# Kernel tuning notes

Measured on AMD Instinct MI355X. Metric: run time of the kernel, lower is better.

Reference implementation:

```python
import jax, jax.numpy as jnp
import numpy as np

D_MODEL = 128; D_STATE = 64; D_CONV = 4; EXPAND = 2; HEADDIM = 32; NGROUPS = 1
D_INNER = EXPAND * D_MODEL            # 256
NHEADS = D_INNER // HEADDIM           # 8
CONV_DIM = D_INNER + 2 * NGROUPS * D_STATE   # 384 (x, B, C streams)
D_IN_PROJ = 2 * D_INNER + 2 * NGROUPS * D_STATE + NHEADS  # 648 (z, xBC, dt)
EPS = 1e-5


def setup_inputs() -> dict:
    key = jax.random.key(0)
    ks = jax.random.split(key, 8)
    B, L = 8, 4096
    x = jax.random.normal(ks[0], (B, L, D_MODEL), jnp.float32)
    norm_w = jnp.ones((D_MODEL,), jnp.float32)
    in_proj_w = jax.random.normal(ks[1], (D_IN_PROJ, D_MODEL), jnp.float32) * (D_MODEL ** -0.5)
    conv_w = jax.random.normal(ks[2], (CONV_DIM, D_CONV), jnp.float32) * (D_CONV ** -0.5)
    conv_b = jnp.zeros((CONV_DIM,), jnp.float32)
    dt_bias = jax.random.uniform(ks[3], (NHEADS,), jnp.float32, -4.0, -1.0)
    A_log = jnp.log(jax.random.uniform(ks[4], (NHEADS,), jnp.float32, 1.0, 16.0))
    D = jnp.ones((NHEADS,), jnp.float32)
    gnorm_w = jnp.ones((D_INNER,), jnp.float32)
    out_proj_w = jax.random.normal(ks[5], (D_MODEL, D_INNER), jnp.float32) * (D_INNER ** -0.5)
    return dict(x=x, norm_w=norm_w, in_proj_w=in_proj_w, conv_w=conv_w, conv_b=conv_b,
                dt_bias=dt_bias, A_log=A_log, D=D, gnorm_w=gnorm_w, out_proj_w=out_proj_w)


def _rmsnorm(x, w):
    return x * jax.lax.rsqrt(jnp.mean(x * x, axis=-1, keepdims=True) + EPS) * w


def _causal_dw_conv(x, w, b):
    # x: [B,L,C]; w: [C,K]; depthwise causal conv along L
    K = w.shape[1]
    xp = jnp.pad(x, ((0, 0), (K - 1, 0), (0, 0)))
    kern = jnp.transpose(w)[:, None, :]  # [K,1,C] for WIO with groups=C
    out = jax.lax.conv_general_dilated(
        xp, kern, window_strides=(1,), padding='VALID',
        dimension_numbers=('NWC', 'WIO', 'NWC'),
        feature_group_count=w.shape[0])
    return out + b


def _ssm(xh, dt, Bm, Cm, A):
    # xh: [B,L,H,P]; dt: [B,L,H]; Bm, Cm: [B,L,N]; A: [H]
    def step(h, inp):
        x_t, dt_t, B_t, C_t = inp
        dA = jnp.exp(dt_t * A)                                   # [B,H]
        h = h * dA[..., None, None] + (dt_t[..., None] * x_t)[..., None] * B_t[:, None, None, :]
        y = jnp.einsum('bhpn,bn->bhp', h, C_t)
        return h, y
    Bsz, L, H, P = xh.shape
    N = Bm.shape[-1]
    h0 = jnp.zeros((Bsz, H, P, N), xh.dtype)
    xs = (xh.transpose(1, 0, 2, 3), dt.transpose(1, 0, 2),
          Bm.transpose(1, 0, 2), Cm.transpose(1, 0, 2))
    _, ys = jax.lax.scan(step, h0, xs)
    return ys.transpose(1, 0, 2, 3)  # [B,L,H,P]


def reference(x, norm_w, in_proj_w, conv_w, conv_b, dt_bias, A_log, D, gnorm_w, out_proj_w):
    xn = _rmsnorm(x, norm_w)
    zxbcdt = xn @ in_proj_w.T                                    # [B,L,648]
    z, xBC, dt = jnp.split(zxbcdt, [D_INNER, D_INNER + CONV_DIM], axis=-1)
    dt = jax.nn.softplus(dt + dt_bias)                           # [B,L,H]
    xBC = jax.nn.silu(_causal_dw_conv(xBC, conv_w, conv_b))
    xs, Bm, Cm = jnp.split(xBC, [D_INNER, D_INNER + NGROUPS * D_STATE], axis=-1)
    Bsz, L, _ = x.shape
    xh = xs.reshape(Bsz, L, NHEADS, HEADDIM)
    A = -jnp.exp(A_log)                                          # [H]
    y = _ssm(xh, dt, Bm, Cm, A) + D[None, None, :, None] * xh    # D skip per head
    y = y.reshape(Bsz, L, D_INNER)
    y = _rmsnorm(y * jax.nn.silu(z), gnorm_w)                    # gated RMSNorm
    out = y @ out_proj_w.T
    return x + out
```

## Files before the change

### kernel.cpp

```cpp
#include <hip/hip_runtime.h>

#define DM    128
#define DI    256
#define NH    8
#define HD    32
#define NS    64
#define CDIM  384
#define DPROJ 648
#define LSEQ  4096
#define NB    8
#define NTOK  32768
#define LC    64
#define NC    64
#define EPSF  1e-5f
#define LOG2E 1.4426950408889634f

typedef __bf16 bf16;
typedef bf16  bf16x8 __attribute__((ext_vector_type(8)));
typedef bf16  bf16x4 __attribute__((ext_vector_type(4)));
typedef short short8 __attribute__((ext_vector_type(8)));
typedef float f32x4  __attribute__((ext_vector_type(4)));

__device__ __forceinline__ unsigned short f2bfbits(float f) {
    unsigned int u = __float_as_uint(f);
    unsigned int r = u + 0x7FFFu + ((u >> 16) & 1u);
    return (unsigned short)(r >> 16);
}
__device__ __forceinline__ float bfbits2f(unsigned short u) {
    return __uint_as_float(((unsigned int)u) << 16);
}

__global__ __launch_bounds__(256) void k_cast(const float* __restrict__ in,
                                              unsigned short* __restrict__ out, int n) {
    int i = blockIdx.x * 256 + threadIdx.x;
    if (i < n) out[i] = f2bfbits(in[i]);
}

__global__ __launch_bounds__(256) void k_rmsdt(const float* __restrict__ x,
                                               const float* __restrict__ w,
                                               const float* __restrict__ w1,
                                               const float* __restrict__ dtb,
                                               unsigned short* __restrict__ xnb,
                                               float* __restrict__ dtf) {
    __shared__ float Xs[4][132];
    __shared__ float Wd[8][132];
    const int t = threadIdx.x;
    {
        int row = t >> 5, col = (t & 31) * 4;
        *(float4*)&Wd[row][col] = *(const float4*)(w1 + (size_t)(640 + row) * DM + col);
    }
    const int wave = t >> 6, lane = t & 63;
    const size_t row = (size_t)blockIdx.x * 4 + wave;
    const float* xr = x + row * DM + lane * 2;
    float v0 = xr[0], v1 = xr[1];
    float ss = v0 * v0 + v1 * v1;
    #pragma unroll
    for (int o = 32; o; o >>= 1) ss += __shfl_xor(ss, o);
    float r = rsqrtf(ss * (1.0f / DM) + EPSF);
    float o0 = v0 * r * w[lane * 2], o1 = v1 * r * w[lane * 2 + 1];
    Xs[wave][lane * 2] = o0; Xs[wave][lane * 2 + 1] = o1;
    ushort2 ob; ob.x = f2bfbits(o0); ob.y = f2bfbits(o1);
    *(ushort2*)(xnb + row * DM + lane * 2) = ob;
    __syncthreads();
    const int h = lane >> 3, ks = lane & 7;
    float acc = 0.f;
    #pragma unroll
    for (int i = 0; i < 4; i++) {
        float4 xv = *(const float4*)&Xs[wave][ks * 16 + i * 4];
        float4 wv = *(const float4*)&Wd[h][ks * 16 + i * 4];
        acc = fmaf(xv.x, wv.x, acc);
        acc = fmaf(xv.y, wv.y, acc);
        acc = fmaf(xv.z, wv.z, acc);
        acc = fmaf(xv.w, wv.w, acc);
    }
    acc += __shfl_xor(acc, 1);
    acc += __shfl_xor(acc, 2);
    acc += __shfl_xor(acc, 4);
    if (ks == 0) {
        float v = acc + dtb[h];
        dtf[row * NH + h] = (v > 20.f) ? v : log1pf(expf(v));
    }
}

__global__ __launch_bounds__(256) void k_gemm1(const unsigned short* __restrict__ A,
                                               const unsigned short* __restrict__ B,
                                               unsigned short* __restrict__ zb,
                                               unsigned short* __restrict__ xbc) {
    __shared__ bf16 As[64 * 40];
    __shared__ bf16 Bs[64 * 40];
    const int t = threadIdx.x;
    const int m0 = blockIdx.x * 64, n0 = blockIdx.y * 64;
    const int wave = t >> 6, lane = t & 63;
    const int wm = wave >> 1, wn = wave & 1;
    const int fr = lane & 15, fk = (lane >> 4) * 8;
    f32x4 acc[2][2] = {};
    const int r = t >> 2, q = (t & 3) * 8;
    for (int k0 = 0; k0 < DM; k0 += 32) {
        __syncthreads();
        *(short8*)&As[r * 40 + q] = *(const short8*)(A + (size_t)(m0 + r) * DM + k0 + q);
        short8 bv = {};
        if (n0 + r < DPROJ) bv = *(const short8*)(B + (size_t)(n0 + r) * DM + k0 + q);
        *(short8*)&Bs[r * 40 + q] = bv;
        __syncthreads();
        #pragma unroll
        for (int mt = 0; mt < 2; mt++) {
            bf16x8 af = *(const bf16x8*)&As[(wm * 32 + mt * 16 + fr) * 40 + fk];
            #pragma unroll
            for (int nt = 0; nt < 2; nt++) {
                bf16x8 bf = *(const bf16x8*)&Bs[(wn * 32 + nt * 16 + fr) * 40 + fk];
                acc[mt][nt] = __builtin_amdgcn_mfma_f32_16x16x32_bf16(af, bf, acc[mt][nt], 0, 0, 0);
            }
        }
    }
    #pragma unroll
    for (int mt = 0; mt < 2; mt++)
        #pragma unroll
        for (int nt = 0; nt < 2; nt++) {
            int n = n0 + wn * 32 + nt * 16 + fr;
            if (n >= 640) continue;
            #pragma unroll
            for (int rr = 0; rr < 4; rr++) {
                int m = m0 + wm * 32 + mt * 16 + (lane >> 4) * 4 + rr;
                unsigned short v = f2bfbits(acc[mt][nt][rr]);
                if (n < DI) zb[(size_t)m * DI + n] = v;
                else        xbc[(size_t)m * CDIM + (n - 256)] = v;
            }
        }
}

__global__ __launch_bounds__(384) void k_conv(const unsigned short* __restrict__ xbc,
                                              const float* __restrict__ cw,
                                              const float* __restrict__ cb,
                                              unsigned short* __restrict__ xcb) {
    const int c = threadIdx.x;
    const int t0 = blockIdx.x * 64;
    const int l0 = t0 & (LSEQ - 1);
    float4 wv = *(const float4*)(cw + c * 4);
    float bias = cb[c];
    const unsigned short* in = xbc + (size_t)t0 * CDIM + c;
    unsigned short* out = xcb + (size_t)t0 * CDIM + c;
    float h1 = 0.f, h2 = 0.f, h3 = 0.f;
    if (l0) {
        h1 = bfbits2f(in[-CDIM]);
        h2 = bfbits2f(in[-2 * CDIM]);
        h3 = bfbits2f(in[-3 * CDIM]);
    }
    #pragma unroll 4
    for (int t = 0; t < 64; t++) {
        float x0 = bfbits2f(in[(size_t)t * CDIM]);
        float acc = bias;
        acc = fmaf(x0, wv.w, acc);
        acc = fmaf(h1, wv.z, acc);
        acc = fmaf(h2, wv.y, acc);
        acc = fmaf(h3, wv.x, acc);
        float s = acc / (1.f + expf(-acc));
        out[(size_t)t * CDIM] = f2bfbits(s);
        h3 = h2; h2 = h1; h1 = x0;
    }
}

__global__ __launch_bounds__(256, 2) void k_ssd1(const unsigned short* __restrict__ xcb,
                                                 const float* __restrict__ dtf,
                                                 const float* __restrict__ alog,
                                                 unsigned short* __restrict__ hst,
                                                 float* __restrict__ dAp) {
    __shared__ bf16 Wl[4][64 * 72];
    __shared__ bf16 Xl[4][64 * 40];
    __shared__ float wl[4][64];
    const int bh = blockIdx.x >> 4, cg = blockIdx.x & 15;
    const int b = bh >> 3, h = bh & 7;
    const int wave = threadIdx.x >> 6, lane = threadIdx.x & 63;
    const int c = cg * 4 + wave;
    const size_t tok0 = (size_t)b * LSEQ + c * LC;
    const float A = -expf(alog[h]);
    float dt = dtf[(tok0 + lane) * NH + h];
    float q = dt * A * LOG2E;
    #pragma unroll
    for (int o = 1; o <= 32; o <<= 1) {
        float tmp = __shfl_up(q, o);
        if (lane >= o) q += tmp;
    }
    float qL = __shfl(q, 63);
    wl[wave][lane] = exp2f(qL - q) * dt;
    const unsigned short* xrow = xcb + tok0 * CDIM;
    #pragma unroll
    for (int it = 0; it < 4; it++) {
        int f = it * 64 + lane, r = f >> 2, c8 = (f & 3) * 8;
        *(bf16x8*)&Xl[wave][r * 40 + c8] = *(const bf16x8*)(xrow + (size_t)r * CDIM + h * HD + c8);
    }
    #pragma unroll
    for (int it = 0; it < 8; it++) {
        int f = it * 64 + lane, r = f >> 3, c8 = (f & 7) * 8;
        float w = wl[wave][r];
        bf16x8 v = *(const bf16x8*)(xrow + (size_t)r * CDIM + 256 + c8);
        bf16x8 o;
        #pragma unroll
        for (int j = 0; j < 8; j++) o[j] = (bf16)((float)v[j] * w);
        *(bf16x8*)&Wl[wave][r * 72 + c8] = o;
    }
    const int m = lane & 15, ko = lane >> 4;
    f32x4 hacc[4][2] = {};
    #pragma unroll
    for (int kh = 0; kh < 2; kh++) {
        bf16x8 xb[2];
        #pragma unroll
        for (int pi = 0; pi < 2; pi++)
            #pragma unroll
            for (int j = 0; j < 8; j++)
                xb[pi][j] = Xl[wave][(kh * 32 + ko * 8 + j) * 40 + pi * 16 + m];
        #pragma unroll
        for (int ni = 0; ni < 4; ni++) {
            bf16x8 af;
            #pragma unroll
            for (int j = 0; j < 8; j++)
                af[j] = Wl[wave][(kh * 32 + ko * 8 + j) * 72 + ni * 16 + m];
            #pragma unroll
            for (int pi = 0; pi < 2; pi++)
                hacc[ni][pi] = __builtin_amdgcn_mfma_f32_16x16x32_bf16(af, xb[pi], hacc[ni][pi], 0, 0, 0);
        }
    }
    unsigned short* hb = hst + (((size_t)bh * NC + c) << 11);
    #pragma unroll
    for (int ni = 0; ni < 4; ni++)
        #pragma unroll
        for (int pi = 0; pi < 2; pi++)
            #pragma unroll
            for (int r = 0; r < 4; r++)
                hb[(ni * 16 + ko * 4 + r) * 32 + pi * 16 + m] = f2bfbits(hacc[ni][pi][r]);
    if (lane == 0) dAp[(size_t)bh * NC + c] = exp2f(qL);
}

__global__ __launch_bounds__(256) void k_ssm2(unsigned short* __restrict__ hst,
                                              const float* __restrict__ dAp) {
    __shared__ float dl[2][NC];
    const int pr = blockIdx.x >> 3, seg = blockIdx.x & 7;
    const int bh0 = pr * 2, bh1 = pr * 2 + 1;
    const int s = seg * 256 + threadIdx.x;
    if (threadIdx.x < NC) dl[0][threadIdx.x] = dAp[(size_t)bh0 * NC + threadIdx.x];
    else if (threadIdx.x < 2 * NC) dl[1][threadIdx.x - NC] = dAp[(size_t)bh1 * NC + threadIdx.x - NC];
    __syncthreads();
    unsigned short* b0 = hst + ((size_t)bh0 * NC << 11) + s;
    unsigned short* b1 = hst + ((size_t)bh1 * NC << 11) + s;
    float r0 = 0.f, r1 = 0.f;
    float n0 = bfbits2f(b0[0]), n1 = bfbits2f(b1[0]);
    for (int c = 0; c < NC; c++) {
        float t0 = n0, t1 = n1;
        if (c + 1 < NC) {
            n0 = bfbits2f(b0[(size_t)(c + 1) << 11]);
            n1 = bfbits2f(b1[(size_t)(c + 1) << 11]);
        }
        b0[(size_t)c << 11] = f2bfbits(r0);
        b1[(size_t)c << 11] = f2bfbits(r1);
        r0 = fmaf(r0, dl[0][c], t0);
        r1 = fmaf(r1, dl[1][c], t1);
    }
}

__global__ __launch_bounds__(256, 2) void k_ssd3(const unsigned short* __restrict__ xcb,
                                                 const float* __restrict__ dtf,
                                                 const float* __restrict__ alog,
                                                 const unsigned short* __restrict__ hst,
                                                 const float* __restrict__ Dw,
                                                 unsigned short* __restrict__ ybb) {
    __shared__ bf16 Pl[4][64 * 72];
    __shared__ bf16 Xl[4][64 * 40];
    __shared__ bf16 Hl[4][64 * 40];
    __shared__ float ql[4][64];
    __shared__ float dl[4][64];
    const int bh = blockIdx.x >> 4, cg = blockIdx.x & 15;
    const int b = bh >> 3, h = bh & 7;
    const int wave = threadIdx.x >> 6, lane = threadIdx.x & 63;
    const int c = cg * 4 + wave;
    const size_t tok0 = (size_t)b * LSEQ + c * LC;
    const float A = -expf(alog[h]);
    const float Dh = Dw[h];
    float dt = dtf[(tok0 + lane) * NH + h];
    float q = dt * A * LOG2E;
    #pragma unroll
    for (int o = 1; o <= 32; o <<= 1) {
        float tmp = __shfl_up(q, o);
        if (lane >= o) q += tmp;
    }
    ql[wave][lane] = q;
    dl[wave][lane] = dt;
    const unsigned short* xrow = xcb + tok0 * CDIM;
    #pragma unroll
    for (int it = 0; it < 4; it++) {
        int f = it * 64 + lane, r = f >> 2, c8 = (f & 3) * 8;
        *(bf16x8*)&Xl[wave][r * 40 + c8] = *(const bf16x8*)(xrow + (size_t)r * CDIM + h * HD + c8);
    }
    const unsigned short* hbg = hst + (((size_t)bh * NC + c) << 11);
    #pragma unroll
    for (int it = 0; it < 4; it++) {
        int f = it * 64 + lane, n = f >> 2, p8 = (f & 3) * 8;
        *(bf16x8*)&Hl[wave][n * 40 + p8] = *(const bf16x8*)(hbg + f * 8);
    }
    const int m = lane & 15, ko = lane >> 4;
    bf16x8 cf[4][2];
    #pragma unroll
    for (int ti = 0; ti < 4; ti++)
        #pragma unroll
        for (int kh = 0; kh < 2; kh++)
            cf[ti][kh] = *(const bf16x8*)(xrow + (size_t)(ti * 16 + m) * CDIM + 320 + kh * 32 + ko * 8);
    f32x4 g[4][4] = {};
    #pragma unroll
    for (int kh = 0; kh < 2; kh++) {
        bf16x8 bfg[4];
        #pragma unroll
        for (int si = 0; si < 4; si++)
            bfg[si] = *(const bf16x8*)(xrow + (size_t)(si * 16 + m) * CDIM + 256 + kh * 32 + ko * 8);
        #pragma unroll
        for (int ti = 0; ti < 4; ti++)
            #pragma unroll
            for (int si = 0; si < 4; si++)
                g[ti][si] = __builtin_amdgcn_mfma_f32_16x16x32_bf16(cf[ti][kh], bfg[si], g[ti][si], 0, 0, 0);
    }
    __syncthreads();
    float qt[4][4], et[4][4];
    #pragma unroll
    for (int ti = 0; ti < 4; ti++)
        #pragma unroll
        for (int r = 0; r < 4; r++) {
            float v = ql[wave][ti * 16 + ko * 4 + r];
            qt[ti][r] = v; et[ti][r] = exp2f(v);
        }
    float qs[4], ds[4];
    #pragma unroll
    for (int si = 0; si < 4; si++) {
        qs[si] = ql[wave][si * 16 + m];
        ds[si] = dl[wave][si * 16 + m];
    }
    #pragma unroll
    for (int ti = 0; ti < 4; ti++)
        #pragma unroll
        for (int si = 0; si < 4; si++)
            #pragma unroll
            for (int r = 0; r < 4; r++) {
                int t = ti * 16 + ko * 4 + r, s = si * 16 + m;
                float p = 0.f;
                if (si <= ti) {
                    float w = (s <= t) ? exp2f(qt[ti][r] - qs[si]) * ds[si] : 0.f;
                    p = g[ti][si][r] * w;
                    if (s == t) p += Dh;
                }
                Pl[wave][t * 72 + s] = (bf16)p;
            }
    f32x4 ya[4][2] = {}, ua[4][2] = {};
    #pragma unroll
    for (int kh = 0; kh < 2; kh++) {
        bf16x8 xb[2], hb2[2];
        #pragma unroll
        for (int pi = 0; pi < 2; pi++)
            #pragma unroll
            for (int j = 0; j < 8; j++) {
                int kk = kh * 32 + ko * 8 + j;
                xb[pi][j]  = Xl[wave][kk * 40 + pi * 16 + m];
                hb2[pi][j] = Hl[wave][kk * 40 + pi * 16 + m];
            }
        #pragma unroll
        for (int ti = 0; ti < 4; ti++) {
            bf16x8 pa = *(const bf16x8*)&Pl[wave][(ti * 16 + m) * 72 + kh * 32 + ko * 8];
            #pragma unroll
            for (int pi = 0; pi < 2; pi++) {
                ya[ti][pi] = __builtin_amdgcn_mfma_f32_16x16x32_bf16(pa, xb[pi], ya[ti][pi], 0, 0, 0);
                ua[ti][pi] = __builtin_amdgcn_mfma_f32_16x16x32_bf16(cf[ti][kh], hb2[pi], ua[ti][pi], 0, 0, 0);
            }
        }
    }
    unsigned short* yrow = ybb + tok0 * DI + h * HD;
    #pragma unroll
    for (int ti = 0; ti < 4; ti++)
        #pragma unroll
        for (int pi = 0; pi < 2; pi++)
            #pragma unroll
            for (int r = 0; r < 4; r++) {
                int t = ti * 16 + ko * 4 + r;
                yrow[(size_t)t * DI + pi * 16 + m] =
                    f2bfbits(ya[ti][pi][r] + et[ti][r] * ua[ti][pi][r]);
            }
}

__global__ __launch_bounds__(256, 2) void k_gemm2g(const unsigned short* __restrict__ ybb,
                                                   const unsigned short* __restrict__ zb,
                                                   const float* __restrict__ gw,
                                                   const unsigned short* __restrict__ w2b,
                                                   const float* __restrict__ xin,
                                                   float* __restrict__ out) {
    __shared__ bf16 Ws[128 * 264];
    __shared__ float gwl[256];
    const int t = threadIdx.x;
    #pragma unroll
    for (int i = 0; i < 16; i++) {
        int f = i * 256 + t;
        int n = f >> 5, u = (f & 31) * 8;
        *(bf16x8*)&Ws[n * 264 + u] = *(const bf16x8*)(w2b + (size_t)n * DI + u);
    }
    gwl[t] = gw[t];
    const int wave = t >> 6, lane = t & 63;
    const int fr = lane & 15, ko = lane >> 4;
    const int m0 = blockIdx.x * 64 + wave * 16;
    const size_t rowo = (size_t)(m0 + fr) * DI;
    float ss = 0.f;
    bf16x8 gb[8];
    #pragma unroll
    for (int kk = 0; kk < 8; kk++) {
        int co = kk * 32 + ko * 8;
        bf16x8 yv = *(const bf16x8*)(ybb + rowo + co);
        bf16x8 zv = *(const bf16x8*)(zb + rowo + co);
        #pragma unroll
        for (int j = 0; j < 8; j++) {
            float z = (float)zv[j];
            float g = (float)yv[j] * (z / (1.f + expf(-z)));
            ss += g * g;
            gb[kk][j] = (bf16)g;
        }
    }
    ss += __shfl_xor(ss, 16);
    ss += __shfl_xor(ss, 32);
    const float rs = rsqrtf(ss * (1.0f / DI) + EPSF);
    __syncthreads();
    #pragma unroll
    for (int kk = 0; kk < 8; kk++) {
        int co = kk * 32 + ko * 8;
        #pragma unroll
        for (int j = 0; j < 8; j++)
            gb[kk][j] = (bf16)((float)gb[kk][j] * rs * gwl[co + j]);
    }
    f32x4 acc[8] = {};
    #pragma unroll
    for (int kk = 0; kk < 8; kk++) {
        #pragma unroll
        for (int nt = 0; nt < 8; nt++) {
            bf16x8 bfr = *(const bf16x8*)&Ws[(nt * 16 + fr) * 264 + kk * 32 + ko * 8];
            acc[nt] = __builtin_amdgcn_mfma_f32_16x16x32_bf16(gb[kk], bfr, acc[nt], 0, 0, 0);
        }
    }
    #pragma unroll
    for (int nt = 0; nt < 8; nt++) {
        int n = nt * 16 + fr;
        #pragma unroll
        for (int rr = 0; rr < 4; rr++) {
            int m = m0 + ko * 4 + rr;
            out[(size_t)m * DM + n] = xin[(size_t)m * DM + n] + acc[nt][rr];
        }
    }
}

extern "C" void kernel_launch(void* const* d_in, const int* in_sizes, int n_in,
                              void* d_out, int out_size, void* d_ws, size_t ws_size,
                              hipStream_t stream) {
    const float* x   = (const float*)d_in[0];
    const float* nw  = (const float*)d_in[1];
    const float* w1  = (const float*)d_in[2];
    const float* cw  = (const float*)d_in[3];
    const float* cb  = (const float*)d_in[4];
    const float* dtb = (const float*)d_in[5];
    const float* al  = (const float*)d_in[6];
    const float* Dw  = (const float*)d_in[7];
    const float* gw  = (const float*)d_in[8];
    const float* w2  = (const float*)d_in[9];
    float* out = (float*)d_out;

    float* ws = (float*)d_ws;
    float*  dAp = ws;
    float*  dtf = dAp + NB * NH * NC;
    unsigned short* hst = (unsigned short*)(dtf + (size_t)NTOK * NH);
    unsigned short* zb  = hst + (size_t)NB * NH * NC * 2048;
    unsigned short* xbc = zb + (size_t)NTOK * DI;
    unsigned short* xcb = xbc + (size_t)NTOK * CDIM;
    unsigned short* ybb = xcb + (size_t)NTOK * CDIM;
    unsigned short* w1b = ybb + (size_t)NTOK * DI;
    unsigned short* w2b = w1b + (size_t)DPROJ * DM;
    unsigned short* xnb = ybb;

    k_cast<<<(DPROJ * DM + 255) / 256, 256, 0, stream>>>(w1, w1b, DPROJ * DM);
    k_cast<<<(DM * DI + 255) / 256, 256, 0, stream>>>(w2, w2b, DM * DI);
    k_rmsdt<<<NTOK / 4, 256, 0, stream>>>(x, nw, w1, dtb, xnb, dtf);
    k_gemm1<<<dim3(NTOK / 64, (DPROJ + 63) / 64), 256, 0, stream>>>(xnb, w1b, zb, xbc);
    k_conv<<<NTOK / 64, 384, 0, stream>>>(xbc, cw, cb, xcb);
    k_ssd1<<<NB * NH * (NC / 4), 256, 0, stream>>>(xcb, dtf, al, hst, dAp);
    k_ssm2<<<(NB * NH / 2) * 8, 256, 0, stream>>>(hst, dAp);
    k_ssd3<<<NB * NH * (NC / 4), 256, 0, stream>>>(xcb, dtf, al, hst, Dw, ybb);
    k_gemm2g<<<NTOK / 64, 256, 0, stream>>>(ybb, zb, gw, w2b, x, out);
}
```

Baseline: 193.1 us.

## Emit transposed conv outputs so SSD kernels load MFMA fragments directly

The conv kernel now writes its output in three layouts: a compact B/C token-major buffer, and channel-major (transposed) x and B buffers staged through shared memory. The SSD chunk kernels then load MFMA operands as contiguous vectors straight from global memory, no longer staging through LDS with scalar transposed reads, so ssd1 can raise occupancy. ssd3 computes the transposed Gram matrix so the P tile is written as packed vectors. The two weight-cast launches are merged and gemm1 drops its N-bound checks by launching exactly 10 column tiles. The conv kernel does more work and writes more bytes in exchange.

```diff
diff --git a/kernel.cpp b/kernel.cpp
--- a/kernel.cpp
+++ b/kernel.cpp
@@ -30,10 +30,17 @@
     return __uint_as_float(((unsigned int)u) << 16);
 }
 
-__global__ __launch_bounds__(256) void k_cast(const float* __restrict__ in,
-                                              unsigned short* __restrict__ out, int n) {
+__global__ __launch_bounds__(256) void k_cast2(const float* __restrict__ a,
+                                               const float* __restrict__ b,
+                                               unsigned short* __restrict__ oa,
+                                               unsigned short* __restrict__ ob,
+                                               int na, int nb) {
     int i = blockIdx.x * 256 + threadIdx.x;
-    if (i < n) out[i] = f2bfbits(in[i]);
+    if (i < na) oa[i] = f2bfbits(a[i]);
+    else {
+        int j = i - na;
+        if (j < nb) ob[j] = f2bfbits(b[j]);
+    }
 }
 
 __global__ __launch_bounds__(256) void k_rmsdt(const float* __restrict__ x,
@@ -98,9 +105,7 @@
     for (int k0 = 0; k0 < DM; k0 += 32) {
         __syncthreads();
         *(short8*)&As[r * 40 + q] = *(const short8*)(A + (size_t)(m0 + r) * DM + k0 + q);
-        short8 bv = {};
-        if (n0 + r < DPROJ) bv = *(const short8*)(B + (size_t)(n0 + r) * DM + k0 + q);
-        *(short8*)&Bs[r * 40 + q] = bv;
+        *(short8*)&Bs[r * 40 + q] = *(const short8*)(B + (size_t)(n0 + r) * DM + k0 + q);
         __syncthreads();
         #pragma unroll
         for (int mt = 0; mt < 2; mt++) {
@@ -117,7 +122,6 @@
         #pragma unroll
         for (int nt = 0; nt < 2; nt++) {
             int n = n0 + wn * 32 + nt * 16 + fr;
-            if (n >= 640) continue;
             #pragma unroll
             for (int rr = 0; rr < 4; rr++) {
                 int m = m0 + wm * 32 + mt * 16 + (lane >> 4) * 4 + rr;
@@ -131,21 +135,24 @@
 __global__ __launch_bounds__(384) void k_conv(const unsigned short* __restrict__ xbc,
                                               const float* __restrict__ cw,
                                               const float* __restrict__ cb,
-                                              unsigned short* __restrict__ xcb) {
+                                              unsigned short* __restrict__ bcA,
+                                              unsigned short* __restrict__ xT,
+                                              unsigned short* __restrict__ bT) {
+    __shared__ __align__(16) unsigned short L[320][72];
     const int c = threadIdx.x;
     const int t0 = blockIdx.x * 64;
     const int l0 = t0 & (LSEQ - 1);
     float4 wv = *(const float4*)(cw + c * 4);
     float bias = cb[c];
     const unsigned short* in = xbc + (size_t)t0 * CDIM + c;
-    unsigned short* out = xcb + (size_t)t0 * CDIM + c;
     float h1 = 0.f, h2 = 0.f, h3 = 0.f;
     if (l0) {
         h1 = bfbits2f(in[-CDIM]);
         h2 = bfbits2f(in[-2 * CDIM]);
         h3 = bfbits2f(in[-3 * CDIM]);
     }
-    #pragma unroll 4
+    short8 pk;
+    #pragma unroll 8
     for (int t = 0; t < 64; t++) {
         float x0 = bfbits2f(in[(size_t)t * CDIM]);
         float acc = bias;
@@ -154,19 +161,34 @@
         acc = fmaf(h2, wv.y, acc);
         acc = fmaf(h3, wv.x, acc);
         float s = acc / (1.f + expf(-acc));
-        out[(size_t)t * CDIM] = f2bfbits(s);
+        unsigned short us = f2bfbits(s);
+        if (c >= 256) bcA[(size_t)(t0 + t) * 128 + (c - 256)] = us;
+        pk[t & 7] = (short)us;
+        if (c < 320 && (t & 7) == 7) *(short8*)&L[c][t - 7] = pk;
         h3 = h2; h2 = h1; h1 = x0;
     }
-}
-
-__global__ __launch_bounds__(256, 2) void k_ssd1(const unsigned short* __restrict__ xcb,
+    __syncthreads();
+    #pragma unroll
+    for (int it = 0; it < 7; it++) {
+        int idx = it * 384 + c;
+        if (idx < 2560) {
+            int row = idx >> 3, tc = (idx & 7) * 8;
+            short8 v = *(const short8*)&L[row][tc];
+            unsigned short* dst = (row < 256)
+                ? xT + (size_t)row * NTOK + t0 + tc
+                : bT + (size_t)(row - 256) * NTOK + t0 + tc;
+            *(short8*)dst = v;
+        }
+    }
+}
+
+__global__ __launch_bounds__(256, 4) void k_ssd1(const unsigned short* __restrict__ bT,
+                                                 const unsigned short* __restrict__ xT,
                                                  const float* __restrict__ dtf,
                                                  const float* __restrict__ alog,
                                                  unsigned short* __restrict__ hst,
                                                  float* __restrict__ dAp) {
-    __shared__ bf16 Wl[4][64 * 72];
-    __shared__ bf16 Xl[4][64 * 40];
-    __shared__ float wl[4][64];
+    __shared__ __align__(16) float wl[4][64];
     const int bh = blockIdx.x >> 4, cg = blockIdx.x & 15;
     const int b = bh >> 3, h = bh & 7;
     const int wave = threadIdx.x >> 6, lane = threadIdx.x & 63;
@@ -182,22 +204,8 @@
     }
     float qL = __shfl(q, 63);
     wl[wave][lane] = exp2f(qL - q) * dt;
-    const unsigned short* xrow = xcb + tok0 * CDIM;
-    #pragma unroll
-    for (int it = 0; it < 4; it++) {
-        int f = it * 64 + lane, r = f >> 2, c8 = (f & 3) * 8;
-        *(bf16x8*)&Xl[wave][r * 40 + c8] = *(const bf16x8*)(xrow + (size_t)r * CDIM + h * HD + c8);
-    }
-    #pragma unroll
-    for (int it = 0; it < 8; it++) {
-        int f = it * 64 + lane, r = f >> 3, c8 = (f & 7) * 8;
-        float w = wl[wave][r];
-        bf16x8 v = *(const bf16x8*)(xrow + (size_t)r * CDIM + 256 + c8);
-        bf16x8 o;
-        #pragma unroll
-        for (int j = 0; j < 8; j++) o[j] = (bf16)((float)v[j] * w);
-        *(bf16x8*)&Wl[wave][r * 72 + c8] = o;
-    }
+    if (lane == 0) dAp[(size_t)bh * NC + c] = exp2f(qL);
+    __syncthreads();
     const int m = lane & 15, ko = lane >> 4;
     f32x4 hacc[4][2] = {};
     #pragma unroll
@@ -205,15 +213,17 @@
         bf16x8 xb[2];
         #pragma unroll
         for (int pi = 0; pi < 2; pi++)
-            #pragma unroll
-            for (int j = 0; j < 8; j++)
-                xb[pi][j] = Xl[wave][(kh * 32 + ko * 8 + j) * 40 + pi * 16 + m];
+            xb[pi] = *(const bf16x8*)(xT + (size_t)(h * HD + pi * 16 + m) * NTOK + tok0 + kh * 32 + ko * 8);
+        f32x4 w0 = *(const f32x4*)&wl[wave][kh * 32 + ko * 8];
+        f32x4 w1 = *(const f32x4*)&wl[wave][kh * 32 + ko * 8 + 4];
         #pragma unroll
         for (int ni = 0; ni < 4; ni++) {
+            bf16x8 bv = *(const bf16x8*)(bT + (size_t)(ni * 16 + m) * NTOK + tok0 + kh * 32 + ko * 8);
             bf16x8 af;
             #pragma unroll
-            for (int j = 0; j < 8; j++)
-                af[j] = Wl[wave][(kh * 32 + ko * 8 + j) * 72 + ni * 16 + m];
+            for (int j = 0; j < 4; j++) af[j] = (bf16)((float)bv[j] * w0[j]);
+            #pragma unroll
+            for (int j = 0; j < 4; j++) af[4 + j] = (bf16)((float)bv[4 + j] * w1[j]);
             #pragma unroll
             for (int pi = 0; pi < 2; pi++)
                 hacc[ni][pi] = __builtin_amdgcn_mfma_f32_16x16x32_bf16(af, xb[pi], hacc[ni][pi], 0, 0, 0);
@@ -223,11 +233,12 @@
     #pragma unroll
     for (int ni = 0; ni < 4; ni++)
         #pragma unroll
-        for (int pi = 0; pi < 2; pi++)
-            #pragma unroll
-            for (int r = 0; r < 4; r++)
-                hb[(ni * 16 + ko * 4 + r) * 32 + pi * 16 + m] = f2bfbits(hacc[ni][pi][r]);
-    if (lane == 0) dAp[(size_t)bh * NC + c] = exp2f(qL);
+        for (int pi = 0; pi < 2; pi++) {
+            bf16x4 pv;
+            #pragma unroll
+            for (int r = 0; r < 4; r++) pv[r] = (bf16)hacc[ni][pi][r];
+            *(bf16x4*)(hb + (pi * 16 + m) * 64 + ni * 16 + ko * 4) = pv;
+        }
 }
 
 __global__ __launch_bounds__(256) void k_ssm2(unsigned short* __restrict__ hst,
@@ -256,17 +267,16 @@
     }
 }
 
-__global__ __launch_bounds__(256, 2) void k_ssd3(const unsigned short* __restrict__ xcb,
+__global__ __launch_bounds__(256, 2) void k_ssd3(const unsigned short* __restrict__ bcA,
+                                                 const unsigned short* __restrict__ xT,
                                                  const float* __restrict__ dtf,
                                                  const float* __restrict__ alog,
                                                  const unsigned short* __restrict__ hst,
                                                  const float* __restrict__ Dw,
                                                  unsigned short* __restrict__ ybb) {
-    __shared__ bf16 Pl[4][64 * 72];
-    __shared__ bf16 Xl[4][64 * 40];
-    __shared__ bf16 Hl[4][64 * 40];
-    __shared__ float ql[4][64];
-    __shared__ float dl[4][64];
+    __shared__ __align__(16) bf16 Pl[4][64 * 72];
+    __shared__ __align__(16) float ql[4][64];
+    __shared__ __align__(16) float dl[4][64];
     const int bh = blockIdx.x >> 4, cg = blockIdx.x & 15;
     const int b = bh >> 3, h = bh & 7;
     const int wave = threadIdx.x >> 6, lane = threadIdx.x & 63;
@@ -283,80 +293,71 @@
     }
     ql[wave][lane] = q;
     dl[wave][lane] = dt;
-    const unsigned short* xrow = xcb + tok0 * CDIM;
-    #pragma unroll
-    for (int it = 0; it < 4; it++) {
-        int f = it * 64 + lane, r = f >> 2, c8 = (f & 3) * 8;
-        *(bf16x8*)&Xl[wave][r * 40 + c8] = *(const bf16x8*)(xrow + (size_t)r * CDIM + h * HD + c8);
-    }
-    const unsigned short* hbg = hst + (((size_t)bh * NC + c) << 11);
-    #pragma unroll
-    for (int it = 0; it < 4; it++) {
-        int f = it * 64 + lane, n = f >> 2, p8 = (f & 3) * 8;
-        *(bf16x8*)&Hl[wave][n * 40 + p8] = *(const bf16x8*)(hbg + f * 8);
-    }
     const int m = lane & 15, ko = lane >> 4;
     bf16x8 cf[4][2];
     #pragma unroll
     for (int ti = 0; ti < 4; ti++)
         #pragma unroll
         for (int kh = 0; kh < 2; kh++)
-            cf[ti][kh] = *(const bf16x8*)(xrow + (size_t)(ti * 16 + m) * CDIM + 320 + kh * 32 + ko * 8);
-    f32x4 g[4][4] = {};
+            cf[ti][kh] = *(const bf16x8*)(bcA + (tok0 + ti * 16 + m) * 128 + 64 + kh * 32 + ko * 8);
+    f32x4 gt[4][4] = {};
     #pragma unroll
     for (int kh = 0; kh < 2; kh++) {
         bf16x8 bfg[4];
         #pragma unroll
         for (int si = 0; si < 4; si++)
-            bfg[si] = *(const bf16x8*)(xrow + (size_t)(si * 16 + m) * CDIM + 256 + kh * 32 + ko * 8);
+            bfg[si] = *(const bf16x8*)(bcA + (tok0 + si * 16 + m) * 128 + kh * 32 + ko * 8);
         #pragma unroll
         for (int ti = 0; ti < 4; ti++)
             #pragma unroll
             for (int si = 0; si < 4; si++)
-                g[ti][si] = __builtin_amdgcn_mfma_f32_16x16x32_bf16(cf[ti][kh], bfg[si], g[ti][si], 0, 0, 0);
-    }
-    __syncthreads();
-    float qt[4][4], et[4][4];
-    #pragma unroll
-    for (int ti = 0; ti < 4; ti++)
-        #pragma unroll
-        for (int r = 0; r < 4; r++) {
-            float v = ql[wave][ti * 16 + ko * 4 + r];
-            qt[ti][r] = v; et[ti][r] = exp2f(v);
-        }
-    float qs[4], ds[4];
+                gt[ti][si] = __builtin_amdgcn_mfma_f32_16x16x32_bf16(bfg[si], cf[ti][kh], gt[ti][si], 0, 0, 0);
+    }
+    __syncthreads();
+    float qt[4];
+    #pragma unroll
+    for (int ti = 0; ti < 4; ti++) qt[ti] = ql[wave][ti * 16 + m];
     #pragma unroll
     for (int si = 0; si < 4; si++) {
-        qs[si] = ql[wave][si * 16 + m];
-        ds[si] = dl[wave][si * 16 + m];
-    }
-    #pragma unroll
-    for (int ti = 0; ti < 4; ti++)
-        #pragma unroll
-        for (int si = 0; si < 4; si++)
-            #pragma unroll
-            for (int r = 0; r < 4; r++) {
-                int t = ti * 16 + ko * 4 + r, s = si * 16 + m;
-                float p = 0.f;
-                if (si <= ti) {
-                    float w = (s <= t) ? exp2f(qt[ti][r] - qs[si]) * ds[si] : 0.f;
-                    p = g[ti][si][r] * w;
-                    if (s == t) p += Dh;
+        f32x4 qs = *(const f32x4*)&ql[wave][si * 16 + ko * 4];
+        f32x4 ds = *(const f32x4*)&dl[wave][si * 16 + ko * 4];
+        #pragma unroll
+        for (int ti = 0; ti < 4; ti++) {
+            bf16x4 pv = {};
+            if (si <= ti) {
+                const int t = ti * 16 + m;
+                #pragma unroll
+                for (int r = 0; r < 4; r++) {
+                    int s = si * 16 + ko * 4 + r;
+                    float p = 0.f;
+                    if (s <= t) {
+                        p = exp2f(qt[ti] - qs[r]) * ds[r] * gt[ti][si][r];
+                        if (s == t) p += Dh;
+                    }
+                    pv[r] = (bf16)p;
                 }
-                Pl[wave][t * 72 + s] = (bf16)p;
             }
+            *(bf16x4*)&Pl[wave][(ti * 16 + m) * 72 + si * 16 + ko * 4] = pv;
+        }
+    }
+    __syncthreads();
+    f32x4 et[4];
+    #pragma unroll
+    for (int ti = 0; ti < 4; ti++) {
+        f32x4 qv = *(const f32x4*)&ql[wave][ti * 16 + ko * 4];
+        #pragma unroll
+        for (int r = 0; r < 4; r++) et[ti][r] = exp2f(qv[r]);
+    }
+    const size_t hbase = ((size_t)bh * NC + c) << 11;
     f32x4 ya[4][2] = {}, ua[4][2] = {};
     #pragma unroll
     for (int kh = 0; kh < 2; kh++) {
         bf16x8 xb[2], hb2[2];
         #pragma unroll
-        for (int pi = 0; pi < 2; pi++)
-            #pragma unroll
-            for (int j = 0; j < 8; j++) {
-                int kk = kh * 32 + ko * 8 + j;
-                xb[pi][j]  = Xl[wave][kk * 40 + pi * 16 + m];
-                hb2[pi][j] = Hl[wave][kk * 40 + pi * 16 + m];
-            }
+        for (int pi = 0; pi < 2; pi++) {
+            xb[pi]  = *(const bf16x8*)(xT + (size_t)(h * HD + pi * 16 + m) * NTOK + tok0 + kh * 32 + ko * 8);
+            hb2[pi] = *(const bf16x8*)(hst + hbase + (pi * 16 + m) * 64 + kh * 32 + ko * 8);
+        }
         #pragma unroll
         for (int ti = 0; ti < 4; ti++) {
             bf16x8 pa = *(const bf16x8*)&Pl[wave][(ti * 16 + m) * 72 + kh * 32 + ko * 8];
@@ -467,19 +468,21 @@
     unsigned short* hst = (unsigned short*)(dtf + (size_t)NTOK * NH);
     unsigned short* zb  = hst + (size_t)NB * NH * NC * 2048;
     unsigned short* xbc = zb + (size_t)NTOK * DI;
-    unsigned short* xcb = xbc + (size_t)NTOK * CDIM;
-    unsigned short* ybb = xcb + (size_t)NTOK * CDIM;
+    unsigned short* bcA = xbc + (size_t)NTOK * CDIM;
+    unsigned short* xT  = bcA + (size_t)NTOK * 128;
+    unsigned short* bT  = xT + (size_t)DI * NTOK;
+    unsigned short* ybb = bT + (size_t)64 * NTOK;
     unsigned short* w1b = ybb + (size_t)NTOK * DI;
     unsigned short* w2b = w1b + (size_t)DPROJ * DM;
     unsigned short* xnb = ybb;
 
-    k_cast<<<(DPROJ * DM + 255) / 256, 256, 0, stream>>>(w1, w1b, DPROJ * DM);
-    k_cast<<<(DM * DI + 255) / 256, 256, 0, stream>>>(w2, w2b, DM * DI);
+    k_cast2<<<(DPROJ * DM + DM * DI + 255) / 256, 256, 0, stream>>>(w1, w2, w1b, w2b,
+                                                                    DPROJ * DM, DM * DI);
     k_rmsdt<<<NTOK / 4, 256, 0, stream>>>(x, nw, w1, dtb, xnb, dtf);
-    k_gemm1<<<dim3(NTOK / 64, (DPROJ + 63) / 64), 256, 0, stream>>>(xnb, w1b, zb, xbc);
-    k_conv<<<NTOK / 64, 384, 0, stream>>>(xbc, cw, cb, xcb);
-    k_ssd1<<<NB * NH * (NC / 4), 256, 0, stream>>>(xcb, dtf, al, hst, dAp);
+    k_gemm1<<<dim3(NTOK / 64, 10), 256, 0, stream>>>(xnb, w1b, zb, xbc);
+    k_conv<<<NTOK / 64, 384, 0, stream>>>(xbc, cw, cb, bcA, xT, bT);
+    k_ssd1<<<NB * NH * (NC / 4), 256, 0, stream>>>(bT, xT, dtf, al, hst, dAp);
     k_ssm2<<<(NB * NH / 2) * 8, 256, 0, stream>>>(hst, dAp);
-    k_ssd3<<<NB * NH * (NC / 4), 256, 0, stream>>>(xcb, dtf, al, hst, Dw, ybb);
+    k_ssd3<<<NB * NH * (NC / 4), 256, 0, stream>>>(bcA, xT, dtf, al, hst, Dw, ybb);
     k_gemm2g<<<NTOK / 64, 256, 0, stream>>>(ybb, zb, gw, w2b, x, out);
 }
```

Result: slower. 200.5 us (+3.9%).
